# Optimization experiments

Hardware: AMD Instinct MI355X
Metric: run time of the kernel (lower is better)

The kernel has to match this reference:

```python
import jax, jax.numpy as jnp
import numpy as np

N = 50000
E = 600000
IN_DIM = 128
HID = 128
HEADS = 4
OUT = HID // HEADS  # per-head out channels
R = 2
LAYERS = 2
NEG_SLOPE = 0.2


def _glorot(key, shape):
    fan_in, fan_out = shape[-2], shape[-1]
    lim = jnp.sqrt(6.0 / (fan_in + fan_out))
    return jax.random.uniform(key, shape, jnp.float32, -lim, lim)


def setup_inputs() -> dict:
    key = jax.random.key(0)
    ks = jax.random.split(key, 20)
    x = jax.random.normal(ks[0], (N, IN_DIM), jnp.float32)
    eidx = jax.random.randint(ks[1], (2, E), 0, N, jnp.int64 if jax.config.jax_enable_x64 else jnp.int32)
    etype = jax.random.randint(ks[2], (E,), 0, R, eidx.dtype)
    d = IN_DIM
    params = {}
    ki = 3
    for l in range(LAYERS):
        params[f"W{l}"] = _glorot(ks[ki], (R, d, HID)); ki += 1            # per-relation weight
        params[f"Q{l}"] = _glorot(ks[ki], (HID, HEADS)); ki += 1           # query proj (dim=1)
        params[f"K{l}"] = _glorot(ks[ki], (HID, HEADS)); ki += 1           # key proj
        params[f"cb{l}"] = jnp.zeros((HID,), jnp.float32)                   # conv bias
        params[f"pW{l}"] = _glorot(ks[ki], (HID, HID)); ki += 1            # proj Linear weight [out,in]
        params[f"pb{l}"] = jnp.zeros((HID,), jnp.float32)
        d = HID
    return dict(x=x, eidx=eidx, etype=etype, **params)


def _rgat_conv(h, src, dst, etype, W, Q, K, b):
    # per-relation transform of all nodes: [R, N, HID]
    xw = jnp.einsum('ni,rio->rno', h, W)
    out_j = xw[etype, src]          # [E, HID] source features under edge's relation
    out_i = xw[etype, dst]          # [E, HID] target features under edge's relation
    # additive self-attention, dim=1: alpha [E, HEADS]
    alpha = jax.nn.leaky_relu(out_i @ Q + out_j @ K, NEG_SLOPE)
    # segment softmax over destination nodes (across-relation)
    m = jax.ops.segment_max(alpha, dst, num_segments=N)
    m = jnp.where(jnp.isfinite(m), m, 0.0)
    e = jnp.exp(alpha - m[dst])
    s = jax.ops.segment_sum(e, dst, num_segments=N)
    a = e / (s[dst] + 1e-16)
    # weighted messages and scatter-sum aggregation
    msg = out_j.reshape(E, HEADS, OUT) * a[:, :, None]
    agg = jax.ops.segment_sum(msg.reshape(E, HID), dst, num_segments=N)
    return agg + b


def reference(x, eidx, etype, W0, Q0, K0, cb0, pW0, pb0, W1, Q1, K1, cb1, pW1, pb1):
    src, dst = eidx[0], eidx[1]  # flow source_to_target: aggregate at eidx[1]
    h = x
    for (W, Q, K, cb, pW, pb) in ((W0, Q0, K0, cb0, pW0, pb0), (W1, Q1, K1, cb1, pW1, pb1)):
        h = _rgat_conv(h, src, dst, etype, W, Q, K, cb)
        h = jax.nn.elu(h @ pW.T + pb)
    return h
```

## Files before the change

kernel.cpp:

```cpp
#include <hip/hip_runtime.h>
#include <hip/hip_bf16.h>

typedef __hip_bfloat16 bf16;
typedef short s16x8 __attribute__((ext_vector_type(8)));
typedef float f32x4 __attribute__((ext_vector_type(4)));

#define N_NODES 50000
#define NPAD    50048
#define E_EDGES 600000
#define HID     128
#define HEADS   4
#define SCAN_B  196

__device__ __forceinline__ unsigned short f2bf_bits(float f) {
  unsigned u = __float_as_uint(f);
  u += 0x7fffu + ((u >> 16) & 1u);
  return (unsigned short)(u >> 16);
}
__device__ __forceinline__ float bf2f(unsigned short b) {
  return __uint_as_float(((unsigned)b) << 16);
}
__device__ __forceinline__ float lo_f(unsigned v) { return __uint_as_float(v << 16); }
__device__ __forceinline__ float hi_f(unsigned v) { return __uint_as_float(v & 0xffff0000u); }

__device__ __forceinline__ float lrelu(float v) { return v >= 0.f ? v : 0.2f * v; }

__global__ __launch_bounds__(256) void detect_kernel(const unsigned short* __restrict__ xb,
                                                     const int* __restrict__ ei,
                                                     int* __restrict__ flags) {
  int t = threadIdx.x;
  __shared__ int cnt[2];
  if (t < 2) cnt[t] = 0;
  __syncthreads();
  unsigned short v = xb[2 * t];
  int ex = (v >> 7) & 0xFF;
  if (ex < 119 || ex > 135) atomicAdd(&cnt[0], 1);
  if (ei[2 * t + 1] != 0) atomicAdd(&cnt[1], 1);
  __syncthreads();
  if (t == 0) {
    flags[0] = (cnt[0] > 64) ? 1 : 0;
    flags[1] = (cnt[1] == 0) ? 1 : 0;
  }
}

__global__ __launch_bounds__(256) void zero_int_kernel(int* __restrict__ p, int n) {
  int i = blockIdx.x * 256 + threadIdx.x;
  if (i < n) p[i] = 0;
}

__global__ __launch_bounds__(256) void cvt_idx_hist_kernel(const int* __restrict__ eidx,
                                                           const int* __restrict__ etype,
                                                           int* __restrict__ dstA, int* __restrict__ pk,
                                                           int* __restrict__ deg,
                                                           const int* __restrict__ flags) {
  int e = blockIdx.x * 256 + threadIdx.x;
  if (e >= E_EDGES) return;
  int s, d, r;
  if (flags[1]) {
    const long long* e64 = (const long long*)eidx;
    const long long* t64 = (const long long*)etype;
    s = (int)e64[e]; d = (int)e64[E_EDGES + e]; r = (int)t64[e];
  } else {
    s = eidx[e]; d = eidx[E_EDGES + e]; r = etype[e];
  }
  dstA[e] = d;
  pk[e] = s | (r << 16);
  atomicAdd(&deg[d], 1);
}

__global__ __launch_bounds__(256) void cvt_xb_kernel(const void* __restrict__ src,
                                                     unsigned short* __restrict__ dst, int n,
                                                     const int* __restrict__ flags) {
  int i = blockIdx.x * 256 + threadIdx.x;
  if (i >= n) return;
  if (flags[0]) dst[i] = f2bf_bits(((const float*)src)[i]);
  else          dst[i] = ((const unsigned short*)src)[i];
}

__global__ __launch_bounds__(256) void cvt_wt_kernel(const void* __restrict__ src0,
                                                     const void* __restrict__ src1,
                                                     unsigned short* __restrict__ dst,
                                                     const int* __restrict__ flags) {
  int idx = blockIdx.x * 256 + threadIdx.x;
  if (idx >= 2 * 2 * HID * HID) return;
  int l = idx >> 15, rem = idx & 32767;
  int r = rem >> 14, i = (rem >> 7) & 127, o = rem & 127;
  const void* src = l ? src1 : src0;
  unsigned short b;
  if (flags[0]) b = f2bf_bits(((const float*)src)[rem]);
  else          b = ((const unsigned short*)src)[rem];
  dst[(size_t)l * 2 * HID * HID + ((size_t)r * HID + o) * HID + i] = b;
}

struct P8 { const void* src[8]; int dstoff[8]; int n[8]; };
__global__ __launch_bounds__(256) void cvt_params_kernel(P8 tab, float* __restrict__ base,
                                                         const int* __restrict__ flags) {
  const int f = flags[0];
  for (int k = 0; k < 8; ++k) {
    int n = tab.n[k];
    for (int i = blockIdx.x * 256 + threadIdx.x; i < n; i += gridDim.x * 256) {
      float v = f ? ((const float*)tab.src[k])[i] : bf2f(((const unsigned short*)tab.src[k])[i]);
      base[tab.dstoff[k] + i] = v;
    }
  }
}

__global__ __launch_bounds__(256) void scan1_kernel(const int* __restrict__ deg,
                                                    int* __restrict__ excl,
                                                    int* __restrict__ bsum) {
  __shared__ int sm[256];
  int t = threadIdx.x, i = blockIdx.x * 256 + t;
  int v = (i < NPAD) ? deg[i] : 0;
  sm[t] = v;
  __syncthreads();
#pragma unroll
  for (int off = 1; off < 256; off <<= 1) {
    int add = (t >= off) ? sm[t - off] : 0;
    __syncthreads();
    sm[t] += add;
    __syncthreads();
  }
  if (i < NPAD) excl[i] = sm[t] - v;
  if (t == 255) bsum[blockIdx.x] = sm[255];
}

__global__ __launch_bounds__(256) void scan23_kernel(const int* __restrict__ excl,
                                                     const int* __restrict__ bsum,
                                                     int* __restrict__ rowstart) {
  __shared__ int sm[256];
  int t = threadIdx.x;
  int v = (t < SCAN_B) ? bsum[t] : 0;
  sm[t] = v;
  __syncthreads();
#pragma unroll
  for (int off = 1; off < 256; off <<= 1) {
    int add = (t >= off) ? sm[t - off] : 0;
    __syncthreads();
    sm[t] += add;
    __syncthreads();
  }
  int bpre = (blockIdx.x > 0) ? sm[blockIdx.x - 1] : 0;
  int i = blockIdx.x * 256 + t;
  if (i < NPAD) rowstart[i] = excl[i] + bpre;
  if (i == 0) rowstart[NPAD] = E_EDGES;
}

__global__ __launch_bounds__(256) void scatter_kernel(const int* __restrict__ dstA,
                                                      const int* __restrict__ pk,
                                                      const int* __restrict__ rowstart,
                                                      int* __restrict__ cnt,
                                                      int* __restrict__ eord) {
  int e = blockIdx.x * 256 + threadIdx.x;
  if (e >= E_EDGES) return;
  int d = dstA[e];
  int pos = rowstart[d] + atomicAdd(&cnt[d], 1);
  eord[pos] = pk[e];
}


__global__ __launch_bounds__(256) void gemm_xw_mfma(const unsigned short* __restrict__ hb,
                                                    const unsigned short* __restrict__ Wbt,
                                                    unsigned short* __restrict__ xw) {
  __shared__ unsigned short As[64][136];
  const int t = threadIdx.x;
  const int wave = t >> 6, lane = t & 63;
  const int row0 = blockIdx.x * 64;
  const int r = wave >> 1, colb = (wave & 1) * 64;
  const int lm = lane & 15, q = lane >> 4;
  const unsigned short* Bt = Wbt + (size_t)r * HID * HID;
  s16x8 bfr[4][4];
#pragma unroll
  for (int kc = 0; kc < 4; ++kc) {
    const int ko = kc * 32 + q * 8;
#pragma unroll
    for (int ct = 0; ct < 4; ++ct)
      bfr[kc][ct] = *(const s16x8*)(Bt + (size_t)(colb + ct * 16 + lm) * HID + ko);
  }
  const unsigned short* gsrc = hb + (size_t)row0 * HID;
#pragma unroll
  for (int j = 0; j < 4; ++j) {
    int idx = j * 256 + t;
    *(s16x8*)&As[idx >> 4][(idx & 15) * 8] = *(const s16x8*)(gsrc + idx * 8);
  }
  __syncthreads();
  f32x4 acc[4][4];
#pragma unroll
  for (int a = 0; a < 4; ++a)
#pragma unroll
    for (int b = 0; b < 4; ++b) { f32x4 z = {0.f, 0.f, 0.f, 0.f}; acc[a][b] = z; }
#pragma unroll
  for (int kc = 0; kc < 4; ++kc) {
    const int ko = kc * 32 + q * 8;
#pragma unroll
    for (int rt = 0; rt < 4; ++rt) {
      s16x8 a = *(const s16x8*)&As[rt * 16 + lm][ko];
#pragma unroll
      for (int ct = 0; ct < 4; ++ct)
        acc[rt][ct] = __builtin_amdgcn_mfma_f32_16x16x32_bf16(a, bfr[kc][ct], acc[rt][ct], 0, 0, 0);
    }
  }
#pragma unroll
  for (int rt = 0; rt < 4; ++rt)
#pragma unroll
    for (int i = 0; i < 4; ++i) {
      int row = row0 + rt * 16 + q * 4 + i;
      if (row < N_NODES) {
#pragma unroll
        for (int ct = 0; ct < 4; ++ct) {
          int o = colb + ct * 16 + lm;
          xw[((size_t)r * NPAD + row) * HID + o] = f2bf_bits(acc[rt][ct][i]);
        }
      }
    }
}

__global__ __launch_bounds__(128) void proj_mfma(const unsigned short* __restrict__ aggb,
                                                 const unsigned short* __restrict__ pWTb,
                                                 const float* __restrict__ bo,
                                                 unsigned short* __restrict__ hbout,
                                                 void* __restrict__ dout,
                                                 const int* __restrict__ flags) {
  __shared__ unsigned short As[64][136];
  const int t = threadIdx.x;
  const int wave = t >> 6, lane = t & 63;
  const int row0 = blockIdx.x * 64;
  const int colb = wave * 64;
  const int lm = lane & 15, q = lane >> 4;
  s16x8 bfr[4][4];
#pragma unroll
  for (int kc = 0; kc < 4; ++kc) {
    const int ko = kc * 32 + q * 8;
#pragma unroll
    for (int ct = 0; ct < 4; ++ct)
      bfr[kc][ct] = *(const s16x8*)(pWTb + (size_t)(colb + ct * 16 + lm) * HID + ko);
  }
  const unsigned short* gsrc = aggb + (size_t)row0 * HID;
#pragma unroll
  for (int j = 0; j < 8; ++j) {
    int idx = j * 128 + t;
    *(s16x8*)&As[idx >> 4][(idx & 15) * 8] = *(const s16x8*)(gsrc + idx * 8);
  }
  __syncthreads();
  f32x4 acc[4][4];
#pragma unroll
  for (int a = 0; a < 4; ++a)
#pragma unroll
    for (int b = 0; b < 4; ++b) { f32x4 z = {0.f, 0.f, 0.f, 0.f}; acc[a][b] = z; }
#pragma unroll
  for (int kc = 0; kc < 4; ++kc) {
    const int ko = kc * 32 + q * 8;
#pragma unroll
    for (int rt = 0; rt < 4; ++rt) {
      s16x8 a = *(const s16x8*)&As[rt * 16 + lm][ko];
#pragma unroll
      for (int ct = 0; ct < 4; ++ct)
        acc[rt][ct] = __builtin_amdgcn_mfma_f32_16x16x32_bf16(a, bfr[kc][ct], acc[rt][ct], 0, 0, 0);
    }
  }
  const int f32out = flags[0];
#pragma unroll
  for (int rt = 0; rt < 4; ++rt)
#pragma unroll
    for (int i = 0; i < 4; ++i) {
      int row = row0 + rt * 16 + q * 4 + i;
      if (row < N_NODES) {
#pragma unroll
        for (int ct = 0; ct < 4; ++ct) {
          int o = colb + ct * 16 + lm;
          float v = acc[rt][ct][i] + bo[o];
          v = v > 0.f ? v : expm1f(v);
          size_t idx = (size_t)row * HID + o;
          if (dout) {
            if (f32out) ((float*)dout)[idx] = v;
            else        ((unsigned short*)dout)[idx] = f2bf_bits(v);
          } else {
            hbout[idx] = f2bf_bits(v);
          }
        }
      }
    }
}

__global__ __launch_bounds__(256) void prep_wq_kernel(const unsigned short* __restrict__ Wbt,
                                                      const float* __restrict__ Qf,
                                                      const float* __restrict__ Kf,
                                                      unsigned short* __restrict__ qkt_hi,
                                                      unsigned short* __restrict__ qkt_lo) {
  int idx = blockIdx.x * 256 + threadIdx.x;
  if (idx >= 2 * 2 * HID) return;
  int i = idx & 127, lr = idx >> 7, l = lr >> 1, r = (lr & 1);
  float aq[4] = {0.f, 0.f, 0.f, 0.f}, ak[4] = {0.f, 0.f, 0.f, 0.f};
  const unsigned short* Wb = Wbt + (size_t)lr * HID * HID;
  const float* Qp = Qf + l * HID * HEADS;
  const float* Kp = Kf + l * HID * HEADS;
  for (int j = 0; j < HID; ++j) {
    float w = bf2f(Wb[j * HID + i]);
    float4 q4 = *(const float4*)(Qp + j * 4);
    float4 k4 = *(const float4*)(Kp + j * 4);
    aq[0] += w * q4.x; aq[1] += w * q4.y; aq[2] += w * q4.z; aq[3] += w * q4.w;
    ak[0] += w * k4.x; ak[1] += w * k4.y; ak[2] += w * k4.z; ak[3] += w * k4.w;
  }
  size_t base = (size_t)l * 16 * HID;
#pragma unroll
  for (int h = 0; h < 4; ++h) {
    unsigned short qh = f2bf_bits(aq[h]);
    unsigned short kh = f2bf_bits(ak[h]);
    float qres = aq[h] - bf2f(qh);
    float kres = ak[h] - bf2f(kh);
    qkt_hi[base + (size_t)(r * 4 + h) * HID + i] = qh;
    qkt_lo[base + (size_t)(r * 4 + h) * HID + i] = f2bf_bits(qres);
    qkt_hi[base + (size_t)(8 + r * 4 + h) * HID + i] = kh;
    qkt_lo[base + (size_t)(8 + r * 4 + h) * HID + i] = f2bf_bits(kres);
  }
}

__global__ __launch_bounds__(256) void qk_mfma_kernel(const unsigned short* __restrict__ hb,
                                                      const unsigned short* __restrict__ qkt_hi,
                                                      const unsigned short* __restrict__ qkt_lo,
                                                      float4* __restrict__ qi4,
                                                      float4* __restrict__ kj4) {
  __shared__ float st[4][16][68];
  const int wave = threadIdx.x >> 6, lane = threadIdx.x & 63;
  const int row0 = blockIdx.x * 256 + wave * 64;
  const int lm = lane & 15, q = lane >> 4;
  if (row0 < NPAD) {
    s16x8 bhi[4], blo[4], af[4][4];
#pragma unroll
    for (int kc = 0; kc < 4; ++kc) {
      const int ko = kc * 32 + q * 8;
      bhi[kc] = *(const s16x8*)(qkt_hi + (size_t)lm * HID + ko);
      blo[kc] = *(const s16x8*)(qkt_lo + (size_t)lm * HID + ko);
    }
#pragma unroll
    for (int kc = 0; kc < 4; ++kc) {
      const int ko = kc * 32 + q * 8;
#pragma unroll
      for (int rt = 0; rt < 4; ++rt)
        af[kc][rt] = *(const s16x8*)(hb + (size_t)(row0 + rt * 16 + lm) * HID + ko);
    }
    f32x4 acc[4];
#pragma unroll
    for (int a = 0; a < 4; ++a) { f32x4 z = {0.f, 0.f, 0.f, 0.f}; acc[a] = z; }
#pragma unroll
    for (int kc = 0; kc < 4; ++kc)
#pragma unroll
      for (int rt = 0; rt < 4; ++rt) {
        acc[rt] = __builtin_amdgcn_mfma_f32_16x16x32_bf16(af[kc][rt], bhi[kc], acc[rt], 0, 0, 0);
        acc[rt] = __builtin_amdgcn_mfma_f32_16x16x32_bf16(af[kc][rt], blo[kc], acc[rt], 0, 0, 0);
      }
#pragma unroll
    for (int rt = 0; rt < 4; ++rt)
      *(f32x4*)&st[wave][lm][rt * 16 + q * 4] = acc[rt];
  }
  __syncthreads();
  if (row0 < NPAD) {
    int n = row0 + lane;
    if (n < N_NODES) {
      float4 v;
      v.x = st[wave][0][lane]; v.y = st[wave][1][lane]; v.z = st[wave][2][lane]; v.w = st[wave][3][lane];
      qi4[n] = v;
      v.x = st[wave][4][lane]; v.y = st[wave][5][lane]; v.z = st[wave][6][lane]; v.w = st[wave][7][lane];
      qi4[NPAD + n] = v;
      v.x = st[wave][8][lane]; v.y = st[wave][9][lane]; v.z = st[wave][10][lane]; v.w = st[wave][11][lane];
      kj4[n] = v;
      v.x = st[wave][12][lane]; v.y = st[wave][13][lane]; v.z = st[wave][14][lane]; v.w = st[wave][15][lane];
      kj4[NPAD + n] = v;
    }
  }
}

__global__ __launch_bounds__(256) void edge_fused_kernel(
    const int* __restrict__ rowstart, const int* __restrict__ eord,
    const float4* __restrict__ qi4, const float4* __restrict__ kj4,
    const unsigned short* __restrict__ xw, unsigned short* __restrict__ aggb) {
  __shared__ volatile float wls[4][4][72];
  const int wave = threadIdx.x >> 6, lane = threadIdx.x & 63;
  const int n = blockIdx.x * 4 + wave;
  unsigned* outp = (unsigned*)(aggb + ((size_t)n << 7)) + lane;
  const int start = rowstart[n];
  const int deg = rowstart[n + 1] - start;
  if (deg == 0) { *outp = 0u; return; }
  const int hh = lane >> 4;
  const int ch2 = lane << 1;
  float2 acc = {0.f, 0.f};
  float ssel;
  if (deg <= 64) {
    int p = 0;
    float a0 = -1e30f, a1 = -1e30f, a2 = -1e30f, a3 = -1e30f;
    if (lane < deg) {
      p = eord[start + lane];
      int s = p & 0xffff, r = p >> 16;
      float4 k4 = kj4[r ? (NPAD + s) : s];
      float4 q4 = r ? qi4[NPAD + n] : qi4[n];
      a0 = lrelu(q4.x + k4.x); a1 = lrelu(q4.y + k4.y);
      a2 = lrelu(q4.z + k4.z); a3 = lrelu(q4.w + k4.w);
    }
    float m0 = a0, m1 = a1, m2 = a2, m3 = a3;
#pragma unroll
    for (int off = 32; off > 0; off >>= 1) {
      m0 = fmaxf(m0, __shfl_xor(m0, off)); m1 = fmaxf(m1, __shfl_xor(m1, off));
      m2 = fmaxf(m2, __shfl_xor(m2, off)); m3 = fmaxf(m3, __shfl_xor(m3, off));
    }
    float w0 = 0.f, w1 = 0.f, w2 = 0.f, w3 = 0.f;
    if (lane < deg) {
      w0 = __expf(a0 - m0); w1 = __expf(a1 - m1);
      w2 = __expf(a2 - m2); w3 = __expf(a3 - m3);
    }
    float s0 = w0, s1 = w1, s2 = w2, s3 = w3;
#pragma unroll
    for (int off = 32; off > 0; off >>= 1) {
      s0 += __shfl_xor(s0, off); s1 += __shfl_xor(s1, off);
      s2 += __shfl_xor(s2, off); s3 += __shfl_xor(s3, off);
    }
    ssel = hh == 0 ? s0 : hh == 1 ? s1 : hh == 2 ? s2 : s3;
    wls[wave][0][lane] = w0;
    wls[wave][1][lane] = w1;
    wls[wave][2][lane] = w2;
    wls[wave][3][lane] = w3;
    volatile const float* wrh = &wls[wave][hh][0];
    const int degp = (deg + 7) & ~7;
#pragma unroll 1
    for (int e = 0; e < degp; e += 8) {
      int pp[8];
      unsigned vv[8];
#pragma unroll
      for (int u = 0; u < 8; ++u)
        pp[u] = __builtin_amdgcn_readlane(p, e + u);
#pragma unroll
      for (int u = 0; u < 8; ++u)
        vv[u] = *(const unsigned*)(xw + ((size_t)((pp[u] & 0xffff) + (pp[u] >> 16) * NPAD) << 7) + ch2);
#pragma unroll
      for (int u = 0; u < 8; ++u) {
        float we = wrh[e + u];
        acc.x = fmaf(lo_f(vv[u]), we, acc.x);
        acc.y = fmaf(hi_f(vv[u]), we, acc.y);
      }
    }
  } else {
    const float4 q0 = qi4[n], q1 = qi4[NPAD + n];
    float4 m = make_float4(-1e30f, -1e30f, -1e30f, -1e30f);
    for (int e = start; e < start + deg; ++e) {
      int pe = eord[e];
      int s = pe & 0xffff, r = pe >> 16;
      float4 k4 = kj4[(size_t)r * NPAD + s];
      float4 q4 = r ? q1 : q0;
      m.x = fmaxf(m.x, lrelu(q4.x + k4.x)); m.y = fmaxf(m.y, lrelu(q4.y + k4.y));
      m.z = fmaxf(m.z, lrelu(q4.z + k4.z)); m.w = fmaxf(m.w, lrelu(q4.w + k4.w));
    }
    float4 sv = make_float4(0.f, 0.f, 0.f, 0.f);
    for (int e = start; e < start + deg; ++e) {
      int pe = eord[e];
      int s = pe & 0xffff, r = pe >> 16;
      float4 k4 = kj4[(size_t)r * NPAD + s];
      float4 q4 = r ? q1 : q0;
      float w0 = __expf(lrelu(q4.x + k4.x) - m.x);
      float w1 = __expf(lrelu(q4.y + k4.y) - m.y);
      float w2 = __expf(lrelu(q4.z + k4.z) - m.z);
      float w3 = __expf(lrelu(q4.w + k4.w) - m.w);
      sv.x += w0; sv.y += w1; sv.z += w2; sv.w += w3;
      float we = hh == 0 ? w0 : hh == 1 ? w1 : hh == 2 ? w2 : w3;
      unsigned v = *(const unsigned*)(xw + (((size_t)r * NPAD + s) << 7) + ch2);
      acc.x = fmaf(lo_f(v), we, acc.x);
      acc.y = fmaf(hi_f(v), we, acc.y);
    }
    ssel = hh == 0 ? sv.x : hh == 1 ? sv.y : hh == 2 ? sv.z : sv.w;
  }
  float inv = 1.f / (ssel + 1e-16f);
  *outp = (unsigned)f2bf_bits(acc.x * inv) | ((unsigned)f2bf_bits(acc.y * inv) << 16);
}

__global__ __launch_bounds__(64) void prep_proj_kernel(const void* __restrict__ pW0,
                                                       const void* __restrict__ pW1,
                                                       const float* __restrict__ cbf,
                                                       const float* __restrict__ pbf,
                                                       unsigned short* __restrict__ pWTb2,
                                                       float* __restrict__ bo2,
                                                       const int* __restrict__ flags) {
  int o = blockIdx.x & 127, l = blockIdx.x >> 7, t = threadIdx.x;
  const void* pWraw = l ? pW1 : pW0;
  const float* cb = cbf + l * HID;
  const int f = flags[0];
  float part = 0.f;
#pragma unroll
  for (int i = t; i < HID; i += 64) {
    float w = f ? ((const float*)pWraw)[o * HID + i] : bf2f(((const unsigned short*)pWraw)[o * HID + i]);
    pWTb2[(size_t)l * HID * HID + o * HID + i] = f2bf_bits(w);
    part += cb[i] * w;
  }
#pragma unroll
  for (int off = 32; off > 0; off >>= 1) part += __shfl_xor(part, off);
  if (t == 0) bo2[l * HID + o] = pbf[l * HID + o] + part;
}

extern "C" void kernel_launch(void* const* d_in, const int* in_sizes, int n_in,
                              void* d_out, int out_size, void* d_ws, size_t ws_size,
                              hipStream_t stream) {
  const void* x     = d_in[0];
  const int*  eidx  = (const int*)d_in[1];
  const int*  etype = (const int*)d_in[2];
  const int iW[2] = {3, 9}, iQ[2] = {4, 10}, iK[2] = {5, 11}, icb[2] = {6, 12}, ipW[2] = {7, 13}, ipb[2] = {8, 14};

  float* ws = (float*)d_ws;
  size_t off = 0;
  int*   flags = (int*)(ws + off); off += 16;
  unsigned short* hb   = (unsigned short*)(ws + off); off += (size_t)NPAD * HID / 2;
  unsigned short* xw   = (unsigned short*)(ws + off); off += (size_t)NPAD * HID;
  float* qi   = ws + off; off += (size_t)2 * NPAD * HEADS;
  float* kj   = ws + off; off += (size_t)2 * NPAD * HEADS;
  unsigned short* aggb = (unsigned short*)(ws + off); off += (size_t)NPAD * HID / 2;
  int* dstA = (int*)(ws + off); off += E_EDGES;
  int* pk   = (int*)(ws + off); off += E_EDGES;
  int* eord = (int*)(ws + off); off += E_EDGES;
  int* deg  = (int*)(ws + off); off += NPAD;
  int* cnt  = (int*)(ws + off); off += NPAD;
  int* excl = (int*)(ws + off); off += NPAD;
  int* rowstart = (int*)(ws + off); off += NPAD + 16;
  int* bsum  = (int*)(ws + off); off += 256;
  unsigned short* Wbt   = (unsigned short*)(ws + off); off += (size_t)2 * 2 * HID * HID / 2;
  unsigned short* pWTb2 = (unsigned short*)(ws + off); off += (size_t)2 * HID * HID / 2;
  unsigned short* qkt_hi = (unsigned short*)(ws + off); off += (size_t)2 * 16 * HID / 2;
  unsigned short* qkt_lo = (unsigned short*)(ws + off); off += (size_t)2 * 16 * HID / 2;
  float* Qf  = ws + off; off += 2 * HID * HEADS;
  float* Kf  = ws + off; off += 2 * HID * HEADS;
  float* cbf = ws + off; off += 2 * HID;
  float* pbf = ws + off; off += 2 * HID;
  float* bo2 = ws + off; off += 2 * HID;

  detect_kernel<<<1, 256, 0, stream>>>((const unsigned short*)x, eidx, flags);
  zero_int_kernel<<<(2 * NPAD + 255) / 256, 256, 0, stream>>>(deg, 2 * NPAD);
  cvt_idx_hist_kernel<<<(E_EDGES + 255) / 256, 256, 0, stream>>>(eidx, etype, dstA, pk, deg, flags);
  cvt_xb_kernel<<<(N_NODES * HID + 255) / 256, 256, 0, stream>>>(x, hb, N_NODES * HID, flags);
  cvt_wt_kernel<<<(2 * 2 * HID * HID + 255) / 256, 256, 0, stream>>>(d_in[iW[0]], d_in[iW[1]], Wbt, flags);
  {
    P8 tab;
    float* base = ws;
    for (int l = 0; l < 2; ++l) {
      tab.src[l * 4 + 0] = d_in[iQ[l]];  tab.dstoff[l * 4 + 0] = (int)(Qf - base) + l * HID * HEADS;  tab.n[l * 4 + 0] = HID * HEADS;
      tab.src[l * 4 + 1] = d_in[iK[l]];  tab.dstoff[l * 4 + 1] = (int)(Kf - base) + l * HID * HEADS;  tab.n[l * 4 + 1] = HID * HEADS;
      tab.src[l * 4 + 2] = d_in[icb[l]]; tab.dstoff[l * 4 + 2] = (int)(cbf - base) + l * HID;         tab.n[l * 4 + 2] = HID;
      tab.src[l * 4 + 3] = d_in[ipb[l]]; tab.dstoff[l * 4 + 3] = (int)(pbf - base) + l * HID;         tab.n[l * 4 + 3] = HID;
    }
    cvt_params_kernel<<<2, 256, 0, stream>>>(tab, base, flags);
  }

  scan1_kernel<<<SCAN_B, 256, 0, stream>>>(deg, excl, bsum);
  scan23_kernel<<<SCAN_B, 256, 0, stream>>>(excl, bsum, rowstart);
  scatter_kernel<<<(E_EDGES + 255) / 256, 256, 0, stream>>>(dstA, pk, rowstart, cnt, eord);

  prep_wq_kernel<<<2, 256, 0, stream>>>(Wbt, Qf, Kf, qkt_hi, qkt_lo);
  prep_proj_kernel<<<2 * HID, 64, 0, stream>>>(d_in[ipW[0]], d_in[ipW[1]], cbf, pbf, pWTb2, bo2, flags);

  const int RB = NPAD / 64;
  const int QB = (NPAD + 255) / 256;
  for (int l = 0; l < 2; ++l) {
    gemm_xw_mfma<<<RB, 256, 0, stream>>>(hb, Wbt + (size_t)l * 2 * HID * HID, xw);
    qk_mfma_kernel<<<QB, 256, 0, stream>>>(hb, qkt_hi + (size_t)l * 16 * HID, qkt_lo + (size_t)l * 16 * HID,
                                           (float4*)qi, (float4*)kj);
    edge_fused_kernel<<<N_NODES / 4, 256, 0, stream>>>(rowstart, eord, (const float4*)qi, (const float4*)kj, xw, aggb);
    proj_mfma<<<RB, 128, 0, stream>>>(aggb, pWTb2 + (size_t)l * HID * HID, bo2 + l * HID, hb,
                                      (l == 1) ? d_out : nullptr, flags);
  }
}
```

Before: 372.1 us.

## Fuse detect/zero kernels, vectorize x conversion, drop softmax max pass, widen gather unroll

Merges the format-detection kernel with the degree-zeroing kernel to save a launch. Vectorizes the fp32-to-bf16 input conversion to process eight elements per thread. In the edge kernel, replaces the max-subtracted softmax with a clamped exp that skips the warp max reduction, and doubles the gather unroll from 8 to 16 edges for more loads in flight. The clamp at 85 changes numerics if logits differ widely, and the wider unroll raises register use and padding waste on low-degree nodes.

```diff
diff --git a/kernel.cpp b/kernel.cpp
--- a/kernel.cpp
+++ b/kernel.cpp
@@ -23,29 +23,29 @@
 __device__ __forceinline__ float lo_f(unsigned v) { return __uint_as_float(v << 16); }
 __device__ __forceinline__ float hi_f(unsigned v) { return __uint_as_float(v & 0xffff0000u); }
 
-__device__ __forceinline__ float lrelu(float v) { return v >= 0.f ? v : 0.2f * v; }
-
-__global__ __launch_bounds__(256) void detect_kernel(const unsigned short* __restrict__ xb,
-                                                     const int* __restrict__ ei,
-                                                     int* __restrict__ flags) {
+__device__ __forceinline__ float lrelu(float v) { return fmaxf(v, 0.2f * v); }
+
+__global__ __launch_bounds__(256) void detect_zero_kernel(const unsigned short* __restrict__ xb,
+                                                          const int* __restrict__ ei,
+                                                          int* __restrict__ flags,
+                                                          int* __restrict__ zp, int nz) {
   int t = threadIdx.x;
-  __shared__ int cnt[2];
-  if (t < 2) cnt[t] = 0;
-  __syncthreads();
-  unsigned short v = xb[2 * t];
-  int ex = (v >> 7) & 0xFF;
-  if (ex < 119 || ex > 135) atomicAdd(&cnt[0], 1);
-  if (ei[2 * t + 1] != 0) atomicAdd(&cnt[1], 1);
-  __syncthreads();
-  if (t == 0) {
-    flags[0] = (cnt[0] > 64) ? 1 : 0;
-    flags[1] = (cnt[1] == 0) ? 1 : 0;
-  }
-}
-
-__global__ __launch_bounds__(256) void zero_int_kernel(int* __restrict__ p, int n) {
-  int i = blockIdx.x * 256 + threadIdx.x;
-  if (i < n) p[i] = 0;
+  int i = blockIdx.x * 256 + t;
+  if (i < nz) zp[i] = 0;
+  if (blockIdx.x == 0) {
+    __shared__ int cnt[2];
+    if (t < 2) cnt[t] = 0;
+    __syncthreads();
+    unsigned short v = xb[2 * t];
+    int ex = (v >> 7) & 0xFF;
+    if (ex < 119 || ex > 135) atomicAdd(&cnt[0], 1);
+    if (ei[2 * t + 1] != 0) atomicAdd(&cnt[1], 1);
+    __syncthreads();
+    if (t == 0) {
+      flags[0] = (cnt[0] > 64) ? 1 : 0;
+      flags[1] = (cnt[1] == 0) ? 1 : 0;
+    }
+  }
 }
 
 __global__ __launch_bounds__(256) void cvt_idx_hist_kernel(const int* __restrict__ eidx,
@@ -69,12 +69,22 @@
 }
 
 __global__ __launch_bounds__(256) void cvt_xb_kernel(const void* __restrict__ src,
-                                                     unsigned short* __restrict__ dst, int n,
+                                                     unsigned short* __restrict__ dst, int n8,
                                                      const int* __restrict__ flags) {
   int i = blockIdx.x * 256 + threadIdx.x;
-  if (i >= n) return;
-  if (flags[0]) dst[i] = f2bf_bits(((const float*)src)[i]);
-  else          dst[i] = ((const unsigned short*)src)[i];
+  if (i >= n8) return;
+  if (flags[0]) {
+    const float4* s4 = (const float4*)src;
+    float4 a = s4[2 * i], b = s4[2 * i + 1];
+    s16x8 o;
+    o[0] = (short)f2bf_bits(a.x); o[1] = (short)f2bf_bits(a.y);
+    o[2] = (short)f2bf_bits(a.z); o[3] = (short)f2bf_bits(a.w);
+    o[4] = (short)f2bf_bits(b.x); o[5] = (short)f2bf_bits(b.y);
+    o[6] = (short)f2bf_bits(b.z); o[7] = (short)f2bf_bits(b.w);
+    *(s16x8*)(dst + (size_t)i * 8) = o;
+  } else {
+    *(s16x8*)(dst + (size_t)i * 8) = ((const s16x8*)src)[i];
+  }
 }
 
 __global__ __launch_bounds__(256) void cvt_wt_kernel(const void* __restrict__ src0,
@@ -386,25 +396,16 @@
   float ssel;
   if (deg <= 64) {
     int p = 0;
-    float a0 = -1e30f, a1 = -1e30f, a2 = -1e30f, a3 = -1e30f;
+    float w0 = 0.f, w1 = 0.f, w2 = 0.f, w3 = 0.f;
     if (lane < deg) {
       p = eord[start + lane];
       int s = p & 0xffff, r = p >> 16;
       float4 k4 = kj4[r ? (NPAD + s) : s];
       float4 q4 = r ? qi4[NPAD + n] : qi4[n];
-      a0 = lrelu(q4.x + k4.x); a1 = lrelu(q4.y + k4.y);
-      a2 = lrelu(q4.z + k4.z); a3 = lrelu(q4.w + k4.w);
-    }
-    float m0 = a0, m1 = a1, m2 = a2, m3 = a3;
-#pragma unroll
-    for (int off = 32; off > 0; off >>= 1) {
-      m0 = fmaxf(m0, __shfl_xor(m0, off)); m1 = fmaxf(m1, __shfl_xor(m1, off));
-      m2 = fmaxf(m2, __shfl_xor(m2, off)); m3 = fmaxf(m3, __shfl_xor(m3, off));
-    }
-    float w0 = 0.f, w1 = 0.f, w2 = 0.f, w3 = 0.f;
-    if (lane < deg) {
-      w0 = __expf(a0 - m0); w1 = __expf(a1 - m1);
-      w2 = __expf(a2 - m2); w3 = __expf(a3 - m3);
+      w0 = __expf(fminf(lrelu(q4.x + k4.x), 85.f));
+      w1 = __expf(fminf(lrelu(q4.y + k4.y), 85.f));
+      w2 = __expf(fminf(lrelu(q4.z + k4.z), 85.f));
+      w3 = __expf(fminf(lrelu(q4.w + k4.w), 85.f));
     }
     float s0 = w0, s1 = w1, s2 = w2, s3 = w3;
 #pragma unroll
@@ -418,19 +419,19 @@
     wls[wave][2][lane] = w2;
     wls[wave][3][lane] = w3;
     volatile const float* wrh = &wls[wave][hh][0];
-    const int degp = (deg + 7) & ~7;
+    const int degp = (deg + 15) & ~15;
 #pragma unroll 1
-    for (int e = 0; e < degp; e += 8) {
-      int pp[8];
-      unsigned vv[8];
-#pragma unroll
-      for (int u = 0; u < 8; ++u)
+    for (int e = 0; e < degp; e += 16) {
+      int pp[16];
+      unsigned vv[16];
+#pragma unroll
+      for (int u = 0; u < 16; ++u)
         pp[u] = __builtin_amdgcn_readlane(p, e + u);
 #pragma unroll
-      for (int u = 0; u < 8; ++u)
+      for (int u = 0; u < 16; ++u)
         vv[u] = *(const unsigned*)(xw + ((size_t)((pp[u] & 0xffff) + (pp[u] >> 16) * NPAD) << 7) + ch2);
 #pragma unroll
-      for (int u = 0; u < 8; ++u) {
+      for (int u = 0; u < 16; ++u) {
         float we = wrh[e + u];
         acc.x = fmaf(lo_f(vv[u]), we, acc.x);
         acc.y = fmaf(hi_f(vv[u]), we, acc.y);
@@ -526,10 +527,9 @@
   float* pbf = ws + off; off += 2 * HID;
   float* bo2 = ws + off; off += 2 * HID;
 
-  detect_kernel<<<1, 256, 0, stream>>>((const unsigned short*)x, eidx, flags);
-  zero_int_kernel<<<(2 * NPAD + 255) / 256, 256, 0, stream>>>(deg, 2 * NPAD);
+  detect_zero_kernel<<<(2 * NPAD + 255) / 256, 256, 0, stream>>>((const unsigned short*)x, eidx, flags, deg, 2 * NPAD);
   cvt_idx_hist_kernel<<<(E_EDGES + 255) / 256, 256, 0, stream>>>(eidx, etype, dstA, pk, deg, flags);
-  cvt_xb_kernel<<<(N_NODES * HID + 255) / 256, 256, 0, stream>>>(x, hb, N_NODES * HID, flags);
+  cvt_xb_kernel<<<(N_NODES * HID / 8 + 255) / 256, 256, 0, stream>>>(x, hb, N_NODES * HID / 8, flags);
   cvt_wt_kernel<<<(2 * 2 * HID * HID + 255) / 256, 256, 0, stream>>>(d_in[iW[0]], d_in[iW[1]], Wbt, flags);
   {
     P8 tab;
```

Measured after the change: 372.7 us. About the same (+0.2%).
